# Kernel optimization log

Hardware: AMD Instinct MI355X
Metric: run time of the kernel (lower is better)

The kernel has to match this reference:

```python
import jax, jax.numpy as jnp
import numpy as np

N_NODES = 50000
N_EDGES = 800000
D_IN = 128
D_HID = 128
D_OUT = 1
N_LAYERS = 3


def _sage_conv(x, src, dst, Wl, bl, Wr):
    # PyG SAGEConv (mean aggr): out = lin_l(mean_{j in N(i)} x_j) + lin_r(x_i)
    n = x.shape[0]
    msg = x[src]                                              # [E, F] gather
    s = jax.ops.segment_sum(msg, dst, num_segments=n)         # [N, F]
    cnt = jax.ops.segment_sum(jnp.ones((src.shape[0],), x.dtype), dst, num_segments=n)
    mean = s / jnp.maximum(cnt, 1.0)[:, None]
    return mean @ Wl.T + bl + x @ Wr.T


def setup_inputs() -> dict:
    key = jax.random.key(0)
    ks = jax.random.split(key, 2 + 3 * N_LAYERS + 2)
    x = jax.random.normal(ks[0], (N_NODES, D_IN), dtype=jnp.float32)
    edge_index = jax.random.randint(ks[1], (2, N_EDGES), 0, N_NODES, dtype=jnp.int64)
    inp = {"x": x, "edge_index": edge_index}
    dims_in = [D_IN] + [D_HID] * (N_LAYERS - 1)
    for i in range(N_LAYERS):
        fi = dims_in[i]
        sc = 1.0 / np.sqrt(fi)
        inp[f"Wl{i}"] = jax.random.uniform(ks[2 + 3 * i], (D_HID, fi), jnp.float32, -sc, sc)
        inp[f"bl{i}"] = jax.random.uniform(ks[3 + 3 * i], (D_HID,), jnp.float32, -sc, sc)
        inp[f"Wr{i}"] = jax.random.uniform(ks[4 + 3 * i], (D_HID, fi), jnp.float32, -sc, sc)
    sc = 1.0 / np.sqrt(D_HID)
    inp["Wf"] = jax.random.uniform(ks[-2], (D_OUT, D_HID), jnp.float32, -sc, sc)
    inp["bf"] = jax.random.uniform(ks[-1], (D_OUT,), jnp.float32, -sc, sc)
    return inp


def reference(x, edge_index, Wl0, bl0, Wr0, Wl1, bl1, Wr1, Wl2, bl2, Wr2, Wf, bf):
    src, dst = edge_index[0], edge_index[1]
    h = x
    # dropout is identity in eval mode (F.dropout with training=False)
    for Wl, bl, Wr in ((Wl0, bl0, Wr0), (Wl1, bl1, Wr1), (Wl2, bl2, Wr2)):
        h = jax.nn.relu(_sage_conv(h, src, dst, Wl, bl, Wr))
    return h @ Wf.T + bf
```

## Files before the change

kernel.cpp:

```cpp
#include <hip/hip_runtime.h>
#include <hip/hip_bf16.h>


constexpr int NN = 50000;
constexpr int NE = 800000;
constexpr int NTILE = NN / 16;
constexpr int EPB = 4096;
constexpr int NBLK = (NE + EPB - 1) / EPB;
constexpr int NBUCK = 196;
constexpr int BCAP = 6144;
constexpr int PCAP = 6144;

using bf16x8 = __attribute__((ext_vector_type(8))) short;
using f32x4  = __attribute__((ext_vector_type(4))) float;

__device__ __forceinline__ unsigned short bf16_rne(float f) {
    unsigned u = __float_as_uint(f);
    unsigned r = (u + 0x7FFFu + ((u >> 16) & 1u)) >> 16;
    return (unsigned short)r;
}
__device__ __forceinline__ float bf16_f(unsigned short h) {
    return __uint_as_float(((unsigned)h) << 16);
}
__device__ __forceinline__ unsigned pack_split(float v) {
    unsigned short hi = bf16_rne(v);
    float r = v - bf16_f(hi);
    unsigned short lo = bf16_rne(r);
    return (((unsigned)hi) << 16) | (unsigned)lo;
}


__global__ __launch_bounds__(256) void k_init(float* __restrict__ out,
        const float* __restrict__ bf, int* __restrict__ bcnt,
        unsigned short* __restrict__ hhi) {
    int i = blockIdx.x * blockDim.x + threadIdx.x;
    if (i < NN) out[i] = bf[0];
    if (i < 256) bcnt[i] = 0;
    if (i < 128) hhi[(size_t)NN * 128 + i] = 0;
}


__global__ __launch_bounds__(256) void k_build_buckets(const int* __restrict__ ei,
        int* __restrict__ bcnt, unsigned* __restrict__ packed) {
    __shared__ unsigned stage[EPB];
    __shared__ int h[256];
    __shared__ int cur[256];
    int t = threadIdx.x;
    h[t] = 0;
    __syncthreads();
    int e0 = blockIdx.x * EPB;
    int e1 = e0 + EPB; if (e1 > NE) e1 = NE;
    for (int e = e0 + t; e < e1; e += 256) {
        int s = ei[e];
        int d = ei[NE + e];
        stage[e - e0] = ((unsigned)d << 16) | (unsigned)s;
        atomicAdd(&h[d >> 8], 1);
    }
    __syncthreads();
    if (t < NBUCK) cur[t] = t * BCAP + atomicAdd(&bcnt[t], h[t]);
    __syncthreads();
    for (int e = e0 + t; e < e1; e += 256) {
        unsigned r = stage[e - e0];
        int pos = atomicAdd(&cur[r >> 24], 1);
        packed[pos] = r;
    }
}

__global__ __launch_bounds__(256) void k_bucket_csr(const unsigned* __restrict__ packed,
        const int* __restrict__ bcnt, unsigned short* __restrict__ perm,
        int* __restrict__ cnt, int* __restrict__ row_start) {
    __shared__ unsigned recs[BCAP];
    __shared__ unsigned short outs[PCAP];
    __shared__ int cntL[256];
    __shared__ int ws[4];
    __shared__ int totS;
    int b = blockIdx.x;
    int m = bcnt[b];
    if (m > BCAP) m = BCAP;
    int t = threadIdx.x;
    cntL[t] = 0;
    __syncthreads();
    int lo = b * BCAP;
    for (int i = t; i < m; i += 256) {
        unsigned r = packed[lo + i];
        recs[i] = r;
        atomicAdd(&cntL[(r >> 16) & 255], 1);
    }
    __syncthreads();
    int lane = t & 63, wave = t >> 6;
    int orig = cntL[t];
    int pc = (orig + 7) & ~7;
    int v = pc;
    for (int o = 1; o < 64; o <<= 1) { int u = __shfl_up(v, o); if (lane >= o) v += u; }
    if (lane == 63) ws[wave] = v;
    __syncthreads();
    int off = 0;
    for (int w = 0; w < wave; ++w) off += ws[w];
    int st = v + off - pc;
    int node = b * 256 + t;
    if (node < NN) { cnt[node] = orig; row_start[node] = b * PCAP + st; }
    if (t == 255) totS = st + pc;
    __syncthreads();
    cntL[t] = st;
    __syncthreads();
    for (int i = t; i < m; i += 256) {
        unsigned r = recs[i];
        int pos = atomicAdd(&cntL[(r >> 16) & 255], 1);
        outs[pos] = (unsigned short)(r & 0xFFFFu);
    }
    for (int i = st + orig; i < st + pc; ++i) outs[i] = (unsigned short)NN;
    __syncthreads();
    int totp = totS;
    for (int i = t; i < totp; i += 256)
        perm[b * PCAP + i] = outs[i];
}


__global__ void k_pack_x(const float* __restrict__ x,
                         unsigned short* __restrict__ hhi,
                         unsigned short* __restrict__ hlo) {
    int i = blockIdx.x * blockDim.x + threadIdx.x;
    constexpr int TOT = NN * 128 / 4;
    if (i < TOT) {
        float4 v = ((const float4*)x)[i];
        unsigned p0 = pack_split(v.x), p1 = pack_split(v.y);
        unsigned p2 = pack_split(v.z), p3 = pack_split(v.w);
        uint2 hi, lo;
        hi.x = (p0 >> 16) | (p1 & 0xFFFF0000u);
        hi.y = (p2 >> 16) | (p3 & 0xFFFF0000u);
        lo.x = (p0 & 0xFFFFu) | (p1 << 16);
        lo.y = (p2 & 0xFFFFu) | (p3 << 16);
        ((uint2*)hhi)[i] = hi;
        ((uint2*)hlo)[i] = lo;
    }
}

__global__ void k_pack_w(const float* __restrict__ Wl, const float* __restrict__ Wr,
                         unsigned short* __restrict__ whi, unsigned short* __restrict__ wlo) {
    int i = blockIdx.x * blockDim.x + threadIdx.x;
    if (i < 128 * 256) {
        int c = i >> 8;
        int k = i & 255;
        float v = (k < 128) ? Wl[c * 128 + k] : Wr[c * 128 + (k - 128)];
        unsigned short hi = bf16_rne(v);
        whi[i] = hi;
        wlo[i] = bf16_rne(v - bf16_f(hi));
    }
}

__global__ __launch_bounds__(256) void k_aggregate(const unsigned short* __restrict__ hhi,
        const int* __restrict__ row_start, const int* __restrict__ cnt,
        const unsigned short* __restrict__ perm,
        unsigned short* __restrict__ shi, unsigned short* __restrict__ slo) {
    int wave = __builtin_amdgcn_readfirstlane(threadIdx.x >> 6);
    int lane = threadIdx.x & 63;
    int node = blockIdx.x * 4 + wave;
    if (node >= NN) return;
    int deg = cnt[node];
    int start = row_start[node];
    int h16 = (lane >> 5) << 4;
    int c8  = (lane & 31) << 3;
    const char* base = (const char*)hhi;
    float a0 = 0.f, a1 = 0.f, a2 = 0.f, a3 = 0.f;
    int pdeg = (deg + 7) & ~7;
    const uint4* pp = (const uint4*)(perm + start);
    int j = 0;
    for (; j + 16 <= pdeg; j += 16) {
        uint4 w0 = pp[0], w1 = pp[1]; pp += 2;
        unsigned pw[8] = {w0.x, w0.y, w0.z, w0.w, w1.x, w1.y, w1.z, w1.w};
        uint2 q[8];
#pragma unroll
        for (int u = 0; u < 8; ++u) {
            unsigned src = (pw[u] >> h16) & 0xFFFFu;
            q[u] = *(const uint2*)(base + ((size_t)src << 8) + c8);
        }
#pragma unroll
        for (int u = 0; u < 8; ++u) {
            a0 += __uint_as_float(q[u].x << 16);
            a1 += __uint_as_float(q[u].x & 0xFFFF0000u);
            a2 += __uint_as_float(q[u].y << 16);
            a3 += __uint_as_float(q[u].y & 0xFFFF0000u);
        }
    }
    if (j < pdeg) {
        uint4 w0 = *pp;
        unsigned pw[4] = {w0.x, w0.y, w0.z, w0.w};
        uint2 q[4];
#pragma unroll
        for (int u = 0; u < 4; ++u) {
            unsigned src = (pw[u] >> h16) & 0xFFFFu;
            q[u] = *(const uint2*)(base + ((size_t)src << 8) + c8);
        }
#pragma unroll
        for (int u = 0; u < 4; ++u) {
            a0 += __uint_as_float(q[u].x << 16);
            a1 += __uint_as_float(q[u].x & 0xFFFF0000u);
            a2 += __uint_as_float(q[u].y << 16);
            a3 += __uint_as_float(q[u].y & 0xFFFF0000u);
        }
    }
    a0 += __shfl_xor(a0, 32);
    a1 += __shfl_xor(a1, 32);
    a2 += __shfl_xor(a2, 32);
    a3 += __shfl_xor(a3, 32);
    float inv = 1.0f / (float)(deg > 1 ? deg : 1);
    unsigned p0 = pack_split(a0 * inv);
    unsigned p1 = pack_split(a1 * inv);
    unsigned p2 = pack_split(a2 * inv);
    unsigned p3 = pack_split(a3 * inv);
    if (lane < 32) {
        uint2 hi, lo;
        hi.x = (p0 >> 16) | (p1 & 0xFFFF0000u);
        hi.y = (p2 >> 16) | (p3 & 0xFFFF0000u);
        lo.x = (p0 & 0xFFFFu) | (p1 << 16);
        lo.y = (p2 & 0xFFFFu) | (p3 << 16);
        ((uint2*)shi)[(size_t)node * 32 + lane] = hi;
        ((uint2*)slo)[(size_t)node * 32 + lane] = lo;
    }
}

__global__ __launch_bounds__(256, 2) void k_gemm_ws(
        const unsigned short* __restrict__ Ahi0, const unsigned short* __restrict__ Alo0,
        const unsigned short* __restrict__ Ahi1, const unsigned short* __restrict__ Alo1,
        const unsigned short* __restrict__ Whi, const unsigned short* __restrict__ Wlo,
        const float* __restrict__ bias,
        unsigned short* __restrict__ Ohi, unsigned short* __restrict__ Olo) {
    int wave = __builtin_amdgcn_readfirstlane(threadIdx.x >> 6);
    int lane = threadIdx.x & 63;
    int row = lane & 15;
    int kb = lane >> 4;
    int ct0 = wave * 2;

    bf16x8 bh[2][8], bl[2][8];
#pragma unroll
    for (int c = 0; c < 2; ++c)
#pragma unroll
        for (int kc = 0; kc < 8; ++kc) {
            size_t widx = (size_t)((ct0 + c) * 16 + row) * 256 + kc * 32 + kb * 8;
            bh[c][kc] = *(const bf16x8*)(Whi + widx);
            bl[c][kc] = *(const bf16x8*)(Wlo + widx);
        }
    float b0 = bias[ct0 * 16 + row];
    float b1 = bias[ct0 * 16 + 16 + row];

    for (int t = blockIdx.x; t < NTILE; t += gridDim.x) {
        int n0 = t * 16;
        size_t rb = (size_t)(n0 + row) * 128 + kb * 8;
        bf16x8 ah[8], al[8];
#pragma unroll
        for (int kc = 0; kc < 4; ++kc) {
            ah[kc] = *(const bf16x8*)(Ahi0 + rb + kc * 32);
            al[kc] = *(const bf16x8*)(Alo0 + rb + kc * 32);
        }
#pragma unroll
        for (int kc = 0; kc < 4; ++kc) {
            ah[4 + kc] = *(const bf16x8*)(Ahi1 + rb + kc * 32);
            al[4 + kc] = *(const bf16x8*)(Alo1 + rb + kc * 32);
        }
        f32x4 acc0 = {0.f, 0.f, 0.f, 0.f};
        f32x4 acc1 = {0.f, 0.f, 0.f, 0.f};
#pragma unroll
        for (int kc = 0; kc < 8; ++kc) {
            acc0 = __builtin_amdgcn_mfma_f32_16x16x32_bf16(ah[kc], bh[0][kc], acc0, 0, 0, 0);
            acc0 = __builtin_amdgcn_mfma_f32_16x16x32_bf16(al[kc], bh[0][kc], acc0, 0, 0, 0);
            acc0 = __builtin_amdgcn_mfma_f32_16x16x32_bf16(ah[kc], bl[0][kc], acc0, 0, 0, 0);
            acc1 = __builtin_amdgcn_mfma_f32_16x16x32_bf16(ah[kc], bh[1][kc], acc1, 0, 0, 0);
            acc1 = __builtin_amdgcn_mfma_f32_16x16x32_bf16(al[kc], bh[1][kc], acc1, 0, 0, 0);
            acc1 = __builtin_amdgcn_mfma_f32_16x16x32_bf16(ah[kc], bl[1][kc], acc1, 0, 0, 0);
        }
        __syncthreads();
        int cb0 = ct0 * 16 + row;
#pragma unroll
        for (int r = 0; r < 4; ++r) {
            int n = n0 + kb * 4 + r;
            size_t ro = (size_t)n * 128;
            unsigned p0 = pack_split(fmaxf(acc0[r] + b0, 0.f));
            unsigned p1 = pack_split(fmaxf(acc1[r] + b1, 0.f));
            Ohi[ro + cb0]      = (unsigned short)(p0 >> 16);
            Olo[ro + cb0]      = (unsigned short)(p0 & 0xFFFFu);
            Ohi[ro + cb0 + 16] = (unsigned short)(p1 >> 16);
            Olo[ro + cb0 + 16] = (unsigned short)(p1 & 0xFFFFu);
        }
    }
}

__global__ __launch_bounds__(256, 2) void k_gemm_head(
        const unsigned short* __restrict__ Ahi0, const unsigned short* __restrict__ Alo0,
        const unsigned short* __restrict__ Ahi1, const unsigned short* __restrict__ Alo1,
        const unsigned short* __restrict__ Whi, const unsigned short* __restrict__ Wlo,
        const float* __restrict__ bias, const float* __restrict__ Wf,
        float* __restrict__ out) {
    int wave = __builtin_amdgcn_readfirstlane(threadIdx.x >> 6);
    int lane = threadIdx.x & 63;
    int row = lane & 15;
    int kb = lane >> 4;
    int ct0 = wave * 2;

    bf16x8 bh[2][8], bl[2][8];
#pragma unroll
    for (int c = 0; c < 2; ++c)
#pragma unroll
        for (int kc = 0; kc < 8; ++kc) {
            size_t widx = (size_t)((ct0 + c) * 16 + row) * 256 + kc * 32 + kb * 8;
            bh[c][kc] = *(const bf16x8*)(Whi + widx);
            bl[c][kc] = *(const bf16x8*)(Wlo + widx);
        }
    float b0 = bias[ct0 * 16 + row];
    float b1 = bias[ct0 * 16 + 16 + row];
    float w0 = Wf[ct0 * 16 + row];
    float w1 = Wf[ct0 * 16 + 16 + row];

    for (int t = blockIdx.x; t < NTILE; t += gridDim.x) {
        int n0 = t * 16;
        size_t rb = (size_t)(n0 + row) * 128 + kb * 8;
        bf16x8 ah[8], al[8];
#pragma unroll
        for (int kc = 0; kc < 4; ++kc) {
            ah[kc] = *(const bf16x8*)(Ahi0 + rb + kc * 32);
            al[kc] = *(const bf16x8*)(Alo0 + rb + kc * 32);
        }
#pragma unroll
        for (int kc = 0; kc < 4; ++kc) {
            ah[4 + kc] = *(const bf16x8*)(Ahi1 + rb + kc * 32);
            al[4 + kc] = *(const bf16x8*)(Alo1 + rb + kc * 32);
        }
        f32x4 acc0 = {0.f, 0.f, 0.f, 0.f};
        f32x4 acc1 = {0.f, 0.f, 0.f, 0.f};
#pragma unroll
        for (int kc = 0; kc < 8; ++kc) {
            acc0 = __builtin_amdgcn_mfma_f32_16x16x32_bf16(ah[kc], bh[0][kc], acc0, 0, 0, 0);
            acc0 = __builtin_amdgcn_mfma_f32_16x16x32_bf16(al[kc], bh[0][kc], acc0, 0, 0, 0);
            acc0 = __builtin_amdgcn_mfma_f32_16x16x32_bf16(ah[kc], bl[0][kc], acc0, 0, 0, 0);
            acc1 = __builtin_amdgcn_mfma_f32_16x16x32_bf16(ah[kc], bh[1][kc], acc1, 0, 0, 0);
            acc1 = __builtin_amdgcn_mfma_f32_16x16x32_bf16(al[kc], bh[1][kc], acc1, 0, 0, 0);
            acc1 = __builtin_amdgcn_mfma_f32_16x16x32_bf16(ah[kc], bl[1][kc], acc1, 0, 0, 0);
        }
        float part[4];
#pragma unroll
        for (int r = 0; r < 4; ++r)
            part[r] = fmaxf(acc0[r] + b0, 0.f) * w0 + fmaxf(acc1[r] + b1, 0.f) * w1;
#pragma unroll
        for (int o = 1; o < 16; o <<= 1) {
#pragma unroll
            for (int r = 0; r < 4; ++r) part[r] += __shfl_xor(part[r], o);
        }
        if (row == 0) {
#pragma unroll
            for (int r = 0; r < 4; ++r) atomicAdd(&out[n0 + kb * 4 + r], part[r]);
        }
    }
}

extern "C" void kernel_launch(void* const* d_in, const int* in_sizes, int n_in,
                              void* d_out, int out_size, void* d_ws, size_t ws_size,
                              hipStream_t stream) {
    const float* x   = (const float*)d_in[0];
    const int*   ei  = (const int*)d_in[1];
    const float* Wl0 = (const float*)d_in[2];
    const float* bl0 = (const float*)d_in[3];
    const float* Wr0 = (const float*)d_in[4];
    const float* Wl1 = (const float*)d_in[5];
    const float* bl1 = (const float*)d_in[6];
    const float* Wr1 = (const float*)d_in[7];
    const float* Wl2 = (const float*)d_in[8];
    const float* bl2 = (const float*)d_in[9];
    const float* Wr2 = (const float*)d_in[10];
    const float* Wf  = (const float*)d_in[11];
    const float* bf  = (const float*)d_in[12];
    float* out = (float*)d_out;

    char* p = (char*)d_ws;
    auto alloc = [&](size_t n) { void* r = (void*)p; p += (n + 255) & ~(size_t)255; return r; };
    int*            bcnt      = (int*)alloc(256 * 4);
    int*            cnt       = (int*)alloc((size_t)NN * 4);
    int*            row_start = (int*)alloc((size_t)NN * 4);
    unsigned short* perm      = (unsigned short*)alloc((size_t)NBUCK * PCAP * 2);
    unsigned short* s_hi      = (unsigned short*)alloc((size_t)(NN + 1) * 128 * 2);
    unsigned short* s_lo      = (unsigned short*)alloc((size_t)(NN + 1) * 128 * 2);
    unsigned short* h_hi      = (unsigned short*)alloc((size_t)(NN + 1) * 128 * 2);
    unsigned short* h_lo      = (unsigned short*)alloc((size_t)(NN + 1) * 128 * 2);
    unsigned short* whi       = (unsigned short*)alloc((size_t)3 * 128 * 256 * 2);
    unsigned short* wlo       = (unsigned short*)alloc((size_t)3 * 128 * 256 * 2);
    unsigned*       packed    = (unsigned*)s_hi;

    dim3 b256(256);
    k_init<<<dim3((NN + 255) / 256), b256, 0, stream>>>(out, bf, bcnt, h_hi);
    k_build_buckets<<<dim3(NBLK), b256, 0, stream>>>(ei, bcnt, packed);
    k_bucket_csr<<<dim3(NBUCK), b256, 0, stream>>>(packed, bcnt, perm, cnt, row_start);

    k_pack_x<<<dim3((NN * 128 / 4 + 255) / 256), b256, 0, stream>>>(x, h_hi, h_lo);
    k_pack_w<<<dim3(128), b256, 0, stream>>>(Wl0, Wr0, whi + 0 * 32768, wlo + 0 * 32768);
    k_pack_w<<<dim3(128), b256, 0, stream>>>(Wl1, Wr1, whi + 1 * 32768, wlo + 1 * 32768);
    k_pack_w<<<dim3(128), b256, 0, stream>>>(Wl2, Wr2, whi + 2 * 32768, wlo + 2 * 32768);

    dim3 gAgg((NN + 3) / 4);
    dim3 gGemm(512);

    k_aggregate<<<gAgg, b256, 0, stream>>>(h_hi, row_start, cnt, perm, s_hi, s_lo);
    k_gemm_ws<<<gGemm, b256, 0, stream>>>(s_hi, s_lo, h_hi, h_lo,
                                          whi + 0 * 32768, wlo + 0 * 32768, bl0, h_hi, h_lo);
    k_aggregate<<<gAgg, b256, 0, stream>>>(h_hi, row_start, cnt, perm, s_hi, s_lo);
    k_gemm_ws<<<gGemm, b256, 0, stream>>>(s_hi, s_lo, h_hi, h_lo,
                                          whi + 1 * 32768, wlo + 1 * 32768, bl1, h_hi, h_lo);
    k_aggregate<<<gAgg, b256, 0, stream>>>(h_hi, row_start, cnt, perm, s_hi, s_lo);
    k_gemm_head<<<gGemm, b256, 0, stream>>>(s_hi, s_lo, h_hi, h_lo,
                                            whi + 2 * 32768, wlo + 2 * 32768, bl2, Wf, out);
}
```

Before: 312.9 us.

## Drop aggregate low half, widen gathers, prefetch GEMM tiles, merge pack kernels

Several changes land together. The aggregated mean is now stored only as a bf16 high part, so the s_lo buffer and the MFMAs that consumed it are removed. Each gather now loads 16 bytes per lane, with four edge groups per wave reduced by cross-lane shuffles. The GEMM kernels double-buffer the A-tile loads so the next tile is fetched during the current tile's MFMAs. The x pack is fused into the init kernel and the three weight packs become one launch. Keeping only the high bf16 half of the mean lowers precision of the aggregated term, and the doubled register buffers may reduce occupancy.

```diff
diff --git a/kernel.cpp b/kernel.cpp
--- a/kernel.cpp
+++ b/kernel.cpp
@@ -10,6 +10,7 @@
 constexpr int NBUCK = 196;
 constexpr int BCAP = 6144;
 constexpr int PCAP = 6144;
+constexpr int GGRID = 512;
 
 using bf16x8 = __attribute__((ext_vector_type(8))) short;
 using f32x4  = __attribute__((ext_vector_type(4))) float;
@@ -30,10 +31,24 @@
 }
 
 
-__global__ __launch_bounds__(256) void k_init(float* __restrict__ out,
-        const float* __restrict__ bf, int* __restrict__ bcnt,
-        unsigned short* __restrict__ hhi) {
+__global__ __launch_bounds__(256) void k_packinit(const float* __restrict__ x,
+        unsigned short* __restrict__ hhi, unsigned short* __restrict__ hlo,
+        float* __restrict__ out, const float* __restrict__ bf,
+        int* __restrict__ bcnt) {
     int i = blockIdx.x * blockDim.x + threadIdx.x;
+    constexpr int TOT = NN * 128 / 4;
+    if (i < TOT) {
+        float4 v = ((const float4*)x)[i];
+        unsigned p0 = pack_split(v.x), p1 = pack_split(v.y);
+        unsigned p2 = pack_split(v.z), p3 = pack_split(v.w);
+        uint2 hi, lo;
+        hi.x = (p0 >> 16) | (p1 & 0xFFFF0000u);
+        hi.y = (p2 >> 16) | (p3 & 0xFFFF0000u);
+        lo.x = (p0 & 0xFFFFu) | (p1 << 16);
+        lo.y = (p2 & 0xFFFFu) | (p3 << 16);
+        ((uint2*)hhi)[i] = hi;
+        ((uint2*)hlo)[i] = lo;
+    }
     if (i < NN) out[i] = bf[0];
     if (i < 256) bcnt[i] = 0;
     if (i < 128) hhi[(size_t)NN * 128 + i] = 0;
@@ -116,239 +131,212 @@
 }
 
 
-__global__ void k_pack_x(const float* __restrict__ x,
-                         unsigned short* __restrict__ hhi,
-                         unsigned short* __restrict__ hlo) {
-    int i = blockIdx.x * blockDim.x + threadIdx.x;
-    constexpr int TOT = NN * 128 / 4;
-    if (i < TOT) {
-        float4 v = ((const float4*)x)[i];
-        unsigned p0 = pack_split(v.x), p1 = pack_split(v.y);
-        unsigned p2 = pack_split(v.z), p3 = pack_split(v.w);
-        uint2 hi, lo;
-        hi.x = (p0 >> 16) | (p1 & 0xFFFF0000u);
-        hi.y = (p2 >> 16) | (p3 & 0xFFFF0000u);
-        lo.x = (p0 & 0xFFFFu) | (p1 << 16);
-        lo.y = (p2 & 0xFFFFu) | (p3 << 16);
-        ((uint2*)hhi)[i] = hi;
-        ((uint2*)hlo)[i] = lo;
-    }
-}
-
-__global__ void k_pack_w(const float* __restrict__ Wl, const float* __restrict__ Wr,
-                         unsigned short* __restrict__ whi, unsigned short* __restrict__ wlo) {
-    int i = blockIdx.x * blockDim.x + threadIdx.x;
-    if (i < 128 * 256) {
-        int c = i >> 8;
-        int k = i & 255;
-        float v = (k < 128) ? Wl[c * 128 + k] : Wr[c * 128 + (k - 128)];
-        unsigned short hi = bf16_rne(v);
-        whi[i] = hi;
-        wlo[i] = bf16_rne(v - bf16_f(hi));
-    }
+__global__ __launch_bounds__(256) void k_pack_w3(
+        const float* __restrict__ Wl0, const float* __restrict__ Wr0,
+        const float* __restrict__ Wl1, const float* __restrict__ Wr1,
+        const float* __restrict__ Wl2, const float* __restrict__ Wr2,
+        unsigned short* __restrict__ whi, unsigned short* __restrict__ wlo) {
+    int layer = blockIdx.x >> 7;
+    int i = (blockIdx.x & 127) * 256 + threadIdx.x;
+    const float* Wl = (layer == 0) ? Wl0 : (layer == 1) ? Wl1 : Wl2;
+    const float* Wr = (layer == 0) ? Wr0 : (layer == 1) ? Wr1 : Wr2;
+    int c = i >> 8;
+    int k = i & 255;
+    float v = (k < 128) ? Wl[c * 128 + k] : Wr[c * 128 + (k - 128)];
+    unsigned short hi = bf16_rne(v);
+    whi[layer * 32768 + i] = hi;
+    wlo[layer * 32768 + i] = bf16_rne(v - bf16_f(hi));
 }
 
 __global__ __launch_bounds__(256) void k_aggregate(const unsigned short* __restrict__ hhi,
         const int* __restrict__ row_start, const int* __restrict__ cnt,
         const unsigned short* __restrict__ perm,
-        unsigned short* __restrict__ shi, unsigned short* __restrict__ slo) {
+        unsigned short* __restrict__ shi) {
     int wave = __builtin_amdgcn_readfirstlane(threadIdx.x >> 6);
     int lane = threadIdx.x & 63;
     int node = blockIdx.x * 4 + wave;
     if (node >= NN) return;
     int deg = cnt[node];
     int start = row_start[node];
-    int h16 = (lane >> 5) << 4;
-    int c8  = (lane & 31) << 3;
+    int eg = lane >> 4;
+    int hsh = (eg & 1) << 4;
+    bool egHi = (eg & 2) != 0;
+    int c16 = (lane & 15) << 4;
     const char* base = (const char*)hhi;
-    float a0 = 0.f, a1 = 0.f, a2 = 0.f, a3 = 0.f;
+    float a0=0.f,a1=0.f,a2=0.f,a3=0.f,a4=0.f,a5=0.f,a6=0.f,a7=0.f;
+#define ACC8(q) { a0 += __uint_as_float((q).x << 16); a1 += __uint_as_float((q).x & 0xFFFF0000u); \
+                  a2 += __uint_as_float((q).y << 16); a3 += __uint_as_float((q).y & 0xFFFF0000u); \
+                  a4 += __uint_as_float((q).z << 16); a5 += __uint_as_float((q).z & 0xFFFF0000u); \
+                  a6 += __uint_as_float((q).w << 16); a7 += __uint_as_float((q).w & 0xFFFF0000u); }
+#define GATH(w) (*(const uint4*)(base + ((size_t)(((w) >> hsh) & 0xFFFFu) << 8) + c16))
     int pdeg = (deg + 7) & ~7;
     const uint4* pp = (const uint4*)(perm + start);
     int j = 0;
     for (; j + 16 <= pdeg; j += 16) {
-        uint4 w0 = pp[0], w1 = pp[1]; pp += 2;
-        unsigned pw[8] = {w0.x, w0.y, w0.z, w0.w, w1.x, w1.y, w1.z, w1.w};
-        uint2 q[8];
-#pragma unroll
-        for (int u = 0; u < 8; ++u) {
-            unsigned src = (pw[u] >> h16) & 0xFFFFu;
-            q[u] = *(const uint2*)(base + ((size_t)src << 8) + c8);
+        uint4 P0 = pp[0], P1 = pp[1]; pp += 2;
+        unsigned w0 = egHi ? P0.y : P0.x;
+        unsigned w1 = egHi ? P0.w : P0.z;
+        unsigned w2 = egHi ? P1.y : P1.x;
+        unsigned w3 = egHi ? P1.w : P1.z;
+        uint4 q0 = GATH(w0);
+        uint4 q1 = GATH(w1);
+        uint4 q2 = GATH(w2);
+        uint4 q3 = GATH(w3);
+        ACC8(q0); ACC8(q1); ACC8(q2); ACC8(q3);
+    }
+    if (j < pdeg) {
+        uint4 P0 = *pp;
+        unsigned w0 = egHi ? P0.y : P0.x;
+        unsigned w1 = egHi ? P0.w : P0.z;
+        uint4 q0 = GATH(w0);
+        uint4 q1 = GATH(w1);
+        ACC8(q0); ACC8(q1);
+    }
+#undef GATH
+#undef ACC8
+    a0 += __shfl_xor(a0, 16); a1 += __shfl_xor(a1, 16);
+    a2 += __shfl_xor(a2, 16); a3 += __shfl_xor(a3, 16);
+    a4 += __shfl_xor(a4, 16); a5 += __shfl_xor(a5, 16);
+    a6 += __shfl_xor(a6, 16); a7 += __shfl_xor(a7, 16);
+    a0 += __shfl_xor(a0, 32); a1 += __shfl_xor(a1, 32);
+    a2 += __shfl_xor(a2, 32); a3 += __shfl_xor(a3, 32);
+    a4 += __shfl_xor(a4, 32); a5 += __shfl_xor(a5, 32);
+    a6 += __shfl_xor(a6, 32); a7 += __shfl_xor(a7, 32);
+    float inv = 1.0f / (float)(deg > 1 ? deg : 1);
+    if (eg == 0) {
+        uint4 o;
+        o.x = (unsigned)bf16_rne(a0 * inv) | ((unsigned)bf16_rne(a1 * inv) << 16);
+        o.y = (unsigned)bf16_rne(a2 * inv) | ((unsigned)bf16_rne(a3 * inv) << 16);
+        o.z = (unsigned)bf16_rne(a4 * inv) | ((unsigned)bf16_rne(a5 * inv) << 16);
+        o.w = (unsigned)bf16_rne(a6 * inv) | ((unsigned)bf16_rne(a7 * inv) << 16);
+        ((uint4*)shi)[(size_t)node * 16 + (lane & 15)] = o;
+    }
+}
+
+#define GEMM_PROLOG \
+    int wave = __builtin_amdgcn_readfirstlane(threadIdx.x >> 6); \
+    int lane = threadIdx.x & 63; \
+    int row = lane & 15; \
+    int kb = lane >> 4; \
+    int ct0 = wave * 2; \
+    bf16x8 bh[2][8], bl[2][8]; \
+    _Pragma("unroll") \
+    for (int c = 0; c < 2; ++c) \
+        _Pragma("unroll") \
+        for (int kc = 0; kc < 8; ++kc) { \
+            size_t widx = (size_t)((ct0 + c) * 16 + row) * 256 + kc * 32 + kb * 8; \
+            bh[c][kc] = *(const bf16x8*)(Whi + widx); \
+            bl[c][kc] = *(const bf16x8*)(Wlo + widx); \
+        } \
+    float b0 = bias[ct0 * 16 + row]; \
+    float b1 = bias[ct0 * 16 + 16 + row];
+
+#define LOADT(AS, AH, AL, t) { \
+        size_t rb = (size_t)((t) * 16 + row) * 128 + kb * 8; \
+        _Pragma("unroll") \
+        for (int kc = 0; kc < 4; ++kc) { \
+            AS[kc] = *(const bf16x8*)(Ash + rb + kc * 32); \
+            AH[kc] = *(const bf16x8*)(Ahh + rb + kc * 32); \
+            AL[kc] = *(const bf16x8*)(Ahl + rb + kc * 32); \
+        } }
+
+#define MFMA40(AS, AH, AL) \
+        f32x4 acc0 = {0.f, 0.f, 0.f, 0.f}; \
+        f32x4 acc1 = {0.f, 0.f, 0.f, 0.f}; \
+        _Pragma("unroll") \
+        for (int kc = 0; kc < 4; ++kc) { \
+            acc0 = __builtin_amdgcn_mfma_f32_16x16x32_bf16(AS[kc], bh[0][kc], acc0, 0, 0, 0); \
+            acc0 = __builtin_amdgcn_mfma_f32_16x16x32_bf16(AS[kc], bl[0][kc], acc0, 0, 0, 0); \
+            acc1 = __builtin_amdgcn_mfma_f32_16x16x32_bf16(AS[kc], bh[1][kc], acc1, 0, 0, 0); \
+            acc1 = __builtin_amdgcn_mfma_f32_16x16x32_bf16(AS[kc], bl[1][kc], acc1, 0, 0, 0); \
+        } \
+        _Pragma("unroll") \
+        for (int kc = 0; kc < 4; ++kc) { \
+            acc0 = __builtin_amdgcn_mfma_f32_16x16x32_bf16(AH[kc], bh[0][4 + kc], acc0, 0, 0, 0); \
+            acc0 = __builtin_amdgcn_mfma_f32_16x16x32_bf16(AL[kc], bh[0][4 + kc], acc0, 0, 0, 0); \
+            acc0 = __builtin_amdgcn_mfma_f32_16x16x32_bf16(AH[kc], bl[0][4 + kc], acc0, 0, 0, 0); \
+            acc1 = __builtin_amdgcn_mfma_f32_16x16x32_bf16(AH[kc], bh[1][4 + kc], acc1, 0, 0, 0); \
+            acc1 = __builtin_amdgcn_mfma_f32_16x16x32_bf16(AL[kc], bh[1][4 + kc], acc1, 0, 0, 0); \
+            acc1 = __builtin_amdgcn_mfma_f32_16x16x32_bf16(AH[kc], bl[1][4 + kc], acc1, 0, 0, 0); \
         }
-#pragma unroll
-        for (int u = 0; u < 8; ++u) {
-            a0 += __uint_as_float(q[u].x << 16);
-            a1 += __uint_as_float(q[u].x & 0xFFFF0000u);
-            a2 += __uint_as_float(q[u].y << 16);
-            a3 += __uint_as_float(q[u].y & 0xFFFF0000u);
-        }
-    }
-    if (j < pdeg) {
-        uint4 w0 = *pp;
-        unsigned pw[4] = {w0.x, w0.y, w0.z, w0.w};
-        uint2 q[4];
-#pragma unroll
-        for (int u = 0; u < 4; ++u) {
-            unsigned src = (pw[u] >> h16) & 0xFFFFu;
-            q[u] = *(const uint2*)(base + ((size_t)src << 8) + c8);
-        }
-#pragma unroll
-        for (int u = 0; u < 4; ++u) {
-            a0 += __uint_as_float(q[u].x << 16);
-            a1 += __uint_as_float(q[u].x & 0xFFFF0000u);
-            a2 += __uint_as_float(q[u].y << 16);
-            a3 += __uint_as_float(q[u].y & 0xFFFF0000u);
-        }
-    }
-    a0 += __shfl_xor(a0, 32);
-    a1 += __shfl_xor(a1, 32);
-    a2 += __shfl_xor(a2, 32);
-    a3 += __shfl_xor(a3, 32);
-    float inv = 1.0f / (float)(deg > 1 ? deg : 1);
-    unsigned p0 = pack_split(a0 * inv);
-    unsigned p1 = pack_split(a1 * inv);
-    unsigned p2 = pack_split(a2 * inv);
-    unsigned p3 = pack_split(a3 * inv);
-    if (lane < 32) {
-        uint2 hi, lo;
-        hi.x = (p0 >> 16) | (p1 & 0xFFFF0000u);
-        hi.y = (p2 >> 16) | (p3 & 0xFFFF0000u);
-        lo.x = (p0 & 0xFFFFu) | (p1 << 16);
-        lo.y = (p2 & 0xFFFFu) | (p3 << 16);
-        ((uint2*)shi)[(size_t)node * 32 + lane] = hi;
-        ((uint2*)slo)[(size_t)node * 32 + lane] = lo;
-    }
-}
 
 __global__ __launch_bounds__(256, 2) void k_gemm_ws(
-        const unsigned short* __restrict__ Ahi0, const unsigned short* __restrict__ Alo0,
-        const unsigned short* __restrict__ Ahi1, const unsigned short* __restrict__ Alo1,
+        const unsigned short* __restrict__ Ash,
+        const unsigned short* __restrict__ Ahh, const unsigned short* __restrict__ Ahl,
         const unsigned short* __restrict__ Whi, const unsigned short* __restrict__ Wlo,
         const float* __restrict__ bias,
         unsigned short* __restrict__ Ohi, unsigned short* __restrict__ Olo) {
-    int wave = __builtin_amdgcn_readfirstlane(threadIdx.x >> 6);
-    int lane = threadIdx.x & 63;
-    int row = lane & 15;
-    int kb = lane >> 4;
-    int ct0 = wave * 2;
-
-    bf16x8 bh[2][8], bl[2][8];
-#pragma unroll
-    for (int c = 0; c < 2; ++c)
-#pragma unroll
-        for (int kc = 0; kc < 8; ++kc) {
-            size_t widx = (size_t)((ct0 + c) * 16 + row) * 256 + kc * 32 + kb * 8;
-            bh[c][kc] = *(const bf16x8*)(Whi + widx);
-            bl[c][kc] = *(const bf16x8*)(Wlo + widx);
-        }
-    float b0 = bias[ct0 * 16 + row];
-    float b1 = bias[ct0 * 16 + 16 + row];
-
-    for (int t = blockIdx.x; t < NTILE; t += gridDim.x) {
-        int n0 = t * 16;
-        size_t rb = (size_t)(n0 + row) * 128 + kb * 8;
-        bf16x8 ah[8], al[8];
-#pragma unroll
-        for (int kc = 0; kc < 4; ++kc) {
-            ah[kc] = *(const bf16x8*)(Ahi0 + rb + kc * 32);
-            al[kc] = *(const bf16x8*)(Alo0 + rb + kc * 32);
-        }
-#pragma unroll
-        for (int kc = 0; kc < 4; ++kc) {
-            ah[4 + kc] = *(const bf16x8*)(Ahi1 + rb + kc * 32);
-            al[4 + kc] = *(const bf16x8*)(Alo1 + rb + kc * 32);
-        }
-        f32x4 acc0 = {0.f, 0.f, 0.f, 0.f};
-        f32x4 acc1 = {0.f, 0.f, 0.f, 0.f};
-#pragma unroll
-        for (int kc = 0; kc < 8; ++kc) {
-            acc0 = __builtin_amdgcn_mfma_f32_16x16x32_bf16(ah[kc], bh[0][kc], acc0, 0, 0, 0);
-            acc0 = __builtin_amdgcn_mfma_f32_16x16x32_bf16(al[kc], bh[0][kc], acc0, 0, 0, 0);
-            acc0 = __builtin_amdgcn_mfma_f32_16x16x32_bf16(ah[kc], bl[0][kc], acc0, 0, 0, 0);
-            acc1 = __builtin_amdgcn_mfma_f32_16x16x32_bf16(ah[kc], bh[1][kc], acc1, 0, 0, 0);
-            acc1 = __builtin_amdgcn_mfma_f32_16x16x32_bf16(al[kc], bh[1][kc], acc1, 0, 0, 0);
-            acc1 = __builtin_amdgcn_mfma_f32_16x16x32_bf16(ah[kc], bl[1][kc], acc1, 0, 0, 0);
-        }
-        __syncthreads();
-        int cb0 = ct0 * 16 + row;
-#pragma unroll
-        for (int r = 0; r < 4; ++r) {
-            int n = n0 + kb * 4 + r;
-            size_t ro = (size_t)n * 128;
-            unsigned p0 = pack_split(fmaxf(acc0[r] + b0, 0.f));
-            unsigned p1 = pack_split(fmaxf(acc1[r] + b1, 0.f));
-            Ohi[ro + cb0]      = (unsigned short)(p0 >> 16);
-            Olo[ro + cb0]      = (unsigned short)(p0 & 0xFFFFu);
-            Ohi[ro + cb0 + 16] = (unsigned short)(p1 >> 16);
-            Olo[ro + cb0 + 16] = (unsigned short)(p1 & 0xFFFFu);
-        }
-    }
+    GEMM_PROLOG
+#define STEP(AS, AH, AL, t) { \
+        MFMA40(AS, AH, AL) \
+        __syncthreads();    \
+        int cb0 = ct0 * 16 + row; \
+        _Pragma("unroll") \
+        for (int r = 0; r < 4; ++r) { \
+            size_t ro = (size_t)((t) * 16 + kb * 4 + r) * 128; \
+            unsigned p0 = pack_split(fmaxf(acc0[r] + b0, 0.f)); \
+            unsigned p1 = pack_split(fmaxf(acc1[r] + b1, 0.f)); \
+            Ohi[ro + cb0]      = (unsigned short)(p0 >> 16); \
+            Olo[ro + cb0]      = (unsigned short)(p0 & 0xFFFFu); \
+            Ohi[ro + cb0 + 16] = (unsigned short)(p1 >> 16); \
+            Olo[ro + cb0 + 16] = (unsigned short)(p1 & 0xFFFFu); \
+        } }
+    bf16x8 sA[4], hA[4], lA[4], sB[4], hB[4], lB[4];
+    int t = blockIdx.x;
+    LOADT(sA, hA, lA, t)
+    int tn = t + GGRID;
+    for (;;) {
+        if (tn < NTILE) LOADT(sB, hB, lB, tn)
+        STEP(sA, hA, lA, t)
+        if (tn >= NTILE) break;
+        t = tn; tn += GGRID;
+        if (tn < NTILE) LOADT(sA, hA, lA, tn)
+        STEP(sB, hB, lB, t)
+        if (tn >= NTILE) break;
+        t = tn; tn += GGRID;
+    }
+#undef STEP
 }
 
 __global__ __launch_bounds__(256, 2) void k_gemm_head(
-        const unsigned short* __restrict__ Ahi0, const unsigned short* __restrict__ Alo0,
-        const unsigned short* __restrict__ Ahi1, const unsigned short* __restrict__ Alo1,
+        const unsigned short* __restrict__ Ash,
+        const unsigned short* __restrict__ Ahh, const unsigned short* __restrict__ Ahl,
         const unsigned short* __restrict__ Whi, const unsigned short* __restrict__ Wlo,
         const float* __restrict__ bias, const float* __restrict__ Wf,
         float* __restrict__ out) {
-    int wave = __builtin_amdgcn_readfirstlane(threadIdx.x >> 6);
-    int lane = threadIdx.x & 63;
-    int row = lane & 15;
-    int kb = lane >> 4;
-    int ct0 = wave * 2;
-
-    bf16x8 bh[2][8], bl[2][8];
-#pragma unroll
-    for (int c = 0; c < 2; ++c)
-#pragma unroll
-        for (int kc = 0; kc < 8; ++kc) {
-            size_t widx = (size_t)((ct0 + c) * 16 + row) * 256 + kc * 32 + kb * 8;
-            bh[c][kc] = *(const bf16x8*)(Whi + widx);
-            bl[c][kc] = *(const bf16x8*)(Wlo + widx);
-        }
-    float b0 = bias[ct0 * 16 + row];
-    float b1 = bias[ct0 * 16 + 16 + row];
+    GEMM_PROLOG
     float w0 = Wf[ct0 * 16 + row];
     float w1 = Wf[ct0 * 16 + 16 + row];
-
-    for (int t = blockIdx.x; t < NTILE; t += gridDim.x) {
-        int n0 = t * 16;
-        size_t rb = (size_t)(n0 + row) * 128 + kb * 8;
-        bf16x8 ah[8], al[8];
-#pragma unroll
-        for (int kc = 0; kc < 4; ++kc) {
-            ah[kc] = *(const bf16x8*)(Ahi0 + rb + kc * 32);
-            al[kc] = *(const bf16x8*)(Alo0 + rb + kc * 32);
-        }
-#pragma unroll
-        for (int kc = 0; kc < 4; ++kc) {
-            ah[4 + kc] = *(const bf16x8*)(Ahi1 + rb + kc * 32);
-            al[4 + kc] = *(const bf16x8*)(Alo1 + rb + kc * 32);
-        }
-        f32x4 acc0 = {0.f, 0.f, 0.f, 0.f};
-        f32x4 acc1 = {0.f, 0.f, 0.f, 0.f};
-#pragma unroll
-        for (int kc = 0; kc < 8; ++kc) {
-            acc0 = __builtin_amdgcn_mfma_f32_16x16x32_bf16(ah[kc], bh[0][kc], acc0, 0, 0, 0);
-            acc0 = __builtin_amdgcn_mfma_f32_16x16x32_bf16(al[kc], bh[0][kc], acc0, 0, 0, 0);
-            acc0 = __builtin_amdgcn_mfma_f32_16x16x32_bf16(ah[kc], bl[0][kc], acc0, 0, 0, 0);
-            acc1 = __builtin_amdgcn_mfma_f32_16x16x32_bf16(ah[kc], bh[1][kc], acc1, 0, 0, 0);
-            acc1 = __builtin_amdgcn_mfma_f32_16x16x32_bf16(al[kc], bh[1][kc], acc1, 0, 0, 0);
-            acc1 = __builtin_amdgcn_mfma_f32_16x16x32_bf16(ah[kc], bl[1][kc], acc1, 0, 0, 0);
-        }
-        float part[4];
-#pragma unroll
-        for (int r = 0; r < 4; ++r)
-            part[r] = fmaxf(acc0[r] + b0, 0.f) * w0 + fmaxf(acc1[r] + b1, 0.f) * w1;
-#pragma unroll
-        for (int o = 1; o < 16; o <<= 1) {
-#pragma unroll
-            for (int r = 0; r < 4; ++r) part[r] += __shfl_xor(part[r], o);
-        }
-        if (row == 0) {
-#pragma unroll
-            for (int r = 0; r < 4; ++r) atomicAdd(&out[n0 + kb * 4 + r], part[r]);
-        }
-    }
+#define HSTEP(AS, AH, AL, t) { \
+        MFMA40(AS, AH, AL) \
+        float part[4]; \
+        _Pragma("unroll") \
+        for (int r = 0; r < 4; ++r) \
+            part[r] = fmaxf(acc0[r] + b0, 0.f) * w0 + fmaxf(acc1[r] + b1, 0.f) * w1; \
+        _Pragma("unroll") \
+        for (int o = 1; o < 16; o <<= 1) { \
+            _Pragma("unroll") \
+            for (int r = 0; r < 4; ++r) part[r] += __shfl_xor(part[r], o); \
+        } \
+        if (row == 0) { \
+            _Pragma("unroll") \
+            for (int r = 0; r < 4; ++r) atomicAdd(&out[(t) * 16 + kb * 4 + r], part[r]); \
+        } }
+    bf16x8 sA[4], hA[4], lA[4], sB[4], hB[4], lB[4];
+    int t = blockIdx.x;
+    LOADT(sA, hA, lA, t)
+    int tn = t + GGRID;
+    for (;;) {
+        if (tn < NTILE) LOADT(sB, hB, lB, tn)
+        HSTEP(sA, hA, lA, t)
+        if (tn >= NTILE) break;
+        t = tn; tn += GGRID;
+        if (tn < NTILE) LOADT(sA, hA, lA, tn)
+        HSTEP(sB, hB, lB, t)
+        if (tn >= NTILE) break;
+        t = tn; tn += GGRID;
+    }
+#undef HSTEP
 }
 
 extern "C" void kernel_launch(void* const* d_in, const int* in_sizes, int n_in,
@@ -376,7 +364,6 @@
     int*            row_start = (int*)alloc((size_t)NN * 4);
     unsigned short* perm      = (unsigned short*)alloc((size_t)NBUCK * PCAP * 2);
     unsigned short* s_hi      = (unsigned short*)alloc((size_t)(NN + 1) * 128 * 2);
-    unsigned short* s_lo      = (unsigned short*)alloc((size_t)(NN + 1) * 128 * 2);
     unsigned short* h_hi      = (unsigned short*)alloc((size_t)(NN + 1) * 128 * 2);
     unsigned short* h_lo      = (unsigned short*)alloc((size_t)(NN + 1) * 128 * 2);
     unsigned short* whi       = (unsigned short*)alloc((size_t)3 * 128 * 256 * 2);
@@ -384,25 +371,22 @@
     unsigned*       packed    = (unsigned*)s_hi;
 
     dim3 b256(256);
-    k_init<<<dim3((NN + 255) / 256), b256, 0, stream>>>(out, bf, bcnt, h_hi);
+    k_packinit<<<dim3((NN * 128 / 4 + 255) / 256), b256, 0, stream>>>(
+        x, h_hi, h_lo, out, bf, bcnt);
     k_build_buckets<<<dim3(NBLK), b256, 0, stream>>>(ei, bcnt, packed);
     k_bucket_csr<<<dim3(NBUCK), b256, 0, stream>>>(packed, bcnt, perm, cnt, row_start);
-
-    k_pack_x<<<dim3((NN * 128 / 4 + 255) / 256), b256, 0, stream>>>(x, h_hi, h_lo);
-    k_pack_w<<<dim3(128), b256, 0, stream>>>(Wl0, Wr0, whi + 0 * 32768, wlo + 0 * 32768);
-    k_pack_w<<<dim3(128), b256, 0, stream>>>(Wl1, Wr1, whi + 1 * 32768, wlo + 1 * 32768);
-    k_pack_w<<<dim3(128), b256, 0, stream>>>(Wl2, Wr2, whi + 2 * 32768, wlo + 2 * 32768);
+    k_pack_w3<<<dim3(384), b256, 0, stream>>>(Wl0, Wr0, Wl1, Wr1, Wl2, Wr2, whi, wlo);
 
     dim3 gAgg((NN + 3) / 4);
-    dim3 gGemm(512);
-
-    k_aggregate<<<gAgg, b256, 0, stream>>>(h_hi, row_start, cnt, perm, s_hi, s_lo);
-    k_gemm_ws<<<gGemm, b256, 0, stream>>>(s_hi, s_lo, h_hi, h_lo,
+    dim3 gGemm(GGRID);
+
+    k_aggregate<<<gAgg, b256, 0, stream>>>(h_hi, row_start, cnt, perm, s_hi);
+    k_gemm_ws<<<gGemm, b256, 0, stream>>>(s_hi, h_hi, h_lo,
                                           whi + 0 * 32768, wlo + 0 * 32768, bl0, h_hi, h_lo);
-    k_aggregate<<<gAgg, b256, 0, stream>>>(h_hi, row_start, cnt, perm, s_hi, s_lo);
-    k_gemm_ws<<<gGemm, b256, 0, stream>>>(s_hi, s_lo, h_hi, h_lo,
+    k_aggregate<<<gAgg, b256, 0, stream>>>(h_hi, row_start, cnt, perm, s_hi);
+    k_gemm_ws<<<gGemm, b256, 0, stream>>>(s_hi, h_hi, h_lo,
                                           whi + 1 * 32768, wlo + 1 * 32768, bl1, h_hi, h_lo);
-    k_aggregate<<<gAgg, b256, 0, stream>>>(h_hi, row_start, cnt, perm, s_hi, s_lo);
-    k_gemm_head<<<gGemm, b256, 0, stream>>>(s_hi, s_lo, h_hi, h_lo,
+    k_aggregate<<<gAgg, b256, 0, stream>>>(h_hi, row_start, cnt, perm, s_hi);
+    k_gemm_head<<<gGemm, b256, 0, stream>>>(s_hi, h_hi, h_lo,
                                             whi + 2 * 32768, wlo + 2 * 32768, bl2, Wf, out);
 }
```

After: 284.7 us. 9.0% less time.
